# Kernel tuning notes

Hardware: AMD Instinct MI355X
Metric: run time of the kernel (lower is better)

Reference implementation:

```python
import jax, jax.numpy as jnp
import numpy as np

EMBED = 1024
N_HEAD = 16
B, T = 4, 2048


def setup_inputs() -> dict:
    key = jax.random.key(0)
    k1, k2, k3 = jax.random.split(key, 3)
    x = jax.random.normal(k1, (B, T, EMBED), dtype=jnp.float32)
    w_attn = jax.random.normal(k2, (EMBED, 3 * EMBED), dtype=jnp.float32) * 0.02
    w_proj = jax.random.normal(k3, (EMBED, EMBED), dtype=jnp.float32) * 0.02
    return {"x": x, "w_attn": w_attn, "w_proj": w_proj}


def reference(x, w_attn, w_proj):
    Bv, Tv, C = x.shape
    hd = C // N_HEAD
    qkv = x @ w_attn                      # [B,T,3C] (bias=False)
    q, k, v = jnp.split(qkv, 3, axis=-1)
    # [B,T,C] -> [B,H,T,hd]
    def heads(t):
        return t.reshape(Bv, Tv, N_HEAD, hd).transpose(0, 2, 1, 3)
    q, k, v = heads(q), heads(k), heads(v)
    att = jnp.einsum('bhqd,bhkd->bhqk', q, k) / jnp.sqrt(jnp.float32(hd))
    causal = jnp.tril(jnp.ones((Tv, Tv), dtype=bool))
    att = jnp.where(causal[None, None], att, -jnp.inf)
    att = jax.nn.softmax(att, axis=-1)    # dropout=0 (eval)
    y = jnp.einsum('bhqk,bhkd->bhqd', att, v)
    y = y.transpose(0, 2, 1, 3).reshape(Bv, Tv, C)
    return y @ w_proj
```

## Files before the change

kernel.cpp:

```cpp
#include <hip/hip_runtime.h>
#include <hip/hip_bf16.h>

typedef __attribute__((ext_vector_type(8))) short bf16x8;
typedef __attribute__((ext_vector_type(4))) float f32x4;

#define C1 0.180336880111112f

static __device__ __forceinline__ unsigned short f2bf(float f) {
    union { float f; unsigned int i; } u; u.f = f;
    unsigned int r = u.i + 0x7fffu + ((u.i >> 16) & 1u);
    return (unsigned short)(r >> 16);
}
static __device__ __forceinline__ unsigned int cvt_pk_bf16(float lo, float hi) {
    unsigned int r;
    asm("v_cvt_pk_bf16_f32 %0, %1, %2" : "=v"(r) : "v"(lo), "v"(hi));
    return r;
}

__global__ __launch_bounds__(256)
void prep_kernel(const float* __restrict__ x, const float* __restrict__ wA, const float* __restrict__ wP,
                 unsigned short* __restrict__ xb, unsigned short* __restrict__ wtA,
                 unsigned short* __restrict__ wtP) {
    const int bid = blockIdx.x, tid = threadIdx.x;
    if (bid < 2048) {
        int i0 = bid * 256 + tid;
        #pragma unroll
        for (int it = 0; it < 4; ++it) {
            int i = i0 + it * 524288;
            float4 v = reinterpret_cast<const float4*>(x)[i];
            ushort4 o;
            o.x = f2bf(v.x); o.y = f2bf(v.y); o.z = f2bf(v.z); o.w = f2bf(v.w);
            reinterpret_cast<ushort4*>(xb)[i] = o;
        }
    } else {
        const float* in; unsigned short* out; int R, C, bx, by;
        if (bid < 5120) { int l = bid - 2048; in = wA; out = wtA; R = 1024; C = 3072; bx = l % 96; by = l / 96; }
        else            { int l = bid - 5120; in = wP; out = wtP; R = 1024; C = 1024; bx = l % 32; by = l / 32; }
        __shared__ float tile[32][33];
        const int c0 = bx * 32, r0 = by * 32;
        const int tx = tid & 31, ty = tid >> 5;
        #pragma unroll
        for (int i = 0; i < 32; i += 8)
            tile[ty + i][tx] = in[(size_t)(r0 + ty + i) * C + c0 + tx];
        __syncthreads();
        #pragma unroll
        for (int i = 0; i < 32; i += 8)
            out[(size_t)(c0 + ty + i) * R + r0 + tx] = f2bf(tile[tx][ty + i]);
    }
}

template<int MODE>
__global__ __launch_bounds__(256, 4)
void gemm_bt2(const unsigned short* __restrict__ A,
              const unsigned short* __restrict__ B,
              void* __restrict__ Cout,
              int M, int N, int K) {
    __shared__ unsigned short As[8192];
    __shared__ unsigned short Bs[8192];
    const int tid = threadIdx.x;
    const int wave = tid >> 6, lane = tid & 63;
    const int wr = wave >> 1, wc = wave & 1;
    const int lg = lane >> 4, lr = lane & 15;
    const int m0 = blockIdx.y * 128, n0 = blockIdx.x * 128;

    const int slot = tid * 16;
    const int srow = slot >> 7;
    const int scol = ((slot & 127) ^ ((srow & 7) << 4)) >> 1;
    const int swz = (lr & 7) << 4;

    f32x4 acc[4][4] = {};

    for (int kt = 0; kt < K; kt += 64) {
        #pragma unroll
        for (int i = 0; i < 4; ++i) {
            __builtin_amdgcn_global_load_lds(
                (const __attribute__((address_space(1))) void*)(A + (size_t)(m0 + i * 32 + srow) * K + kt + scol),
                (__attribute__((address_space(3))) void*)(As + ((i * 4096 + slot) >> 1)), 16, 0, 0);
            __builtin_amdgcn_global_load_lds(
                (const __attribute__((address_space(1))) void*)(B + (size_t)(n0 + i * 32 + srow) * K + kt + scol),
                (__attribute__((address_space(3))) void*)(Bs + ((i * 4096 + slot) >> 1)), 16, 0, 0);
        }
        __syncthreads();
        #pragma unroll
        for (int kk = 0; kk < 2; ++kk) {
            bf16x8 af[4], bfr[4];
            #pragma unroll
            for (int mi = 0; mi < 4; ++mi)
                af[mi] = *reinterpret_cast<const bf16x8*>(
                    (const char*)As + (wr * 64 + mi * 16 + lr) * 128 + ((kk * 64 + lg * 16) ^ swz));
            #pragma unroll
            for (int ni = 0; ni < 4; ++ni)
                bfr[ni] = *reinterpret_cast<const bf16x8*>(
                    (const char*)Bs + (wc * 64 + ni * 16 + lr) * 128 + ((kk * 64 + lg * 16) ^ swz));
            #pragma unroll
            for (int mi = 0; mi < 4; ++mi)
                #pragma unroll
                for (int ni = 0; ni < 4; ++ni)
                    acc[mi][ni] = __builtin_amdgcn_mfma_f32_16x16x32_bf16(af[mi], bfr[ni], acc[mi][ni], 0, 0, 0);
        }
        __syncthreads();
    }

    if (MODE == 0) {
        float* C = (float*)Cout;
        #pragma unroll
        for (int mi = 0; mi < 4; ++mi)
            #pragma unroll
            for (int ni = 0; ni < 4; ++ni)
                #pragma unroll
                for (int r = 0; r < 4; ++r) {
                    int row = m0 + wr * 64 + mi * 16 + lg * 4 + r;
                    int col = n0 + wc * 64 + ni * 16 + lr;
                    C[(size_t)row * N + col] = acc[mi][ni][r];
                }
    } else {
        unsigned short* QKV = (unsigned short*)Cout;
        #pragma unroll
        for (int mi = 0; mi < 4; ++mi) {
            int rowb = m0 + wr * 64 + mi * 16 + lg * 4;
            int bb = rowb >> 11, t = rowb & 2047;
            #pragma unroll
            for (int ni = 0; ni < 4; ++ni) {
                int col = n0 + wc * 64 + ni * 16 + lr;
                int which = col >> 10;
                int hh = (col & 1023) >> 6;
                int d = col & 63;
                int bhh = bb * 16 + hh;
                if (which == 2) {
                    ushort4 o;
                    o.x = f2bf(acc[mi][ni][0]); o.y = f2bf(acc[mi][ni][1]);
                    o.z = f2bf(acc[mi][ni][2]); o.w = f2bf(acc[mi][ni][3]);
                    *reinterpret_cast<ushort4*>(QKV + (size_t)2 * 8388608 +
                                                ((size_t)bhh * 64 + d) * 2048 + t) = o;
                } else {
                    #pragma unroll
                    for (int r = 0; r < 4; ++r)
                        QKV[(size_t)which * 8388608 +
                            ((size_t)bhh * 2048 + t + r) * 64 + d] = f2bf(acc[mi][ni][r]);
                }
            }
        }
    }
}

__global__ __launch_bounds__(256)
void attn_fwd(const unsigned short* __restrict__ Qb,
              const unsigned short* __restrict__ Kb,
              const unsigned short* __restrict__ Vtb,
              unsigned short* __restrict__ Yb) {
    const int bh = blockIdx.x;
    const int qt = 15 - (int)blockIdx.y;
    const int tid = threadIdx.x;
    const int wave = tid >> 6, lane = tid & 63;
    const int lg = lane >> 4, lr = lane & 15;
    const int b = bh >> 4, h = bh & 15;

    __shared__ unsigned short Ks[2][4096];
    __shared__ unsigned short Vs[2][4096];
    __shared__ unsigned short Ps[4][32][72];

    const unsigned short* Qh = Qb + (size_t)bh * (2048 * 64);
    const unsigned short* Kh = Kb + (size_t)bh * (2048 * 64);
    const unsigned short* Vh = Vtb + (size_t)bh * (64 * 2048);

    const int slot = tid * 16;
    const int srow = slot >> 7;
    const int scol = ((slot & 127) ^ ((srow & 7) << 4)) >> 1;

    const int swz = (lr & 7) << 4;
    const short one_bf = (short)0x3F80;
    const bf16x8 onesv = {one_bf, one_bf, one_bf, one_bf, one_bf, one_bf, one_bf, one_bf};

#define STAGE(bb, kv)                                                                              \
    {                                                                                              \
        _Pragma("unroll")                                                                          \
        for (int i_ = 0; i_ < 2; ++i_) {                                                           \
            __builtin_amdgcn_global_load_lds(                                                      \
                (const __attribute__((address_space(1))) void*)(Kh + (size_t)((kv) + i_ * 32 + srow) * 64 + scol), \
                (__attribute__((address_space(3))) void*)(Ks[bb] + ((i_ * 4096 + slot) >> 1)), 16, 0, 0); \
            __builtin_amdgcn_global_load_lds(                                                      \
                (const __attribute__((address_space(1))) void*)(Vh + (size_t)(i_ * 32 + srow) * 2048 + (kv) + scol), \
                (__attribute__((address_space(3))) void*)(Vs[bb] + ((i_ * 4096 + slot) >> 1)), 16, 0, 0); \
        }                                                                                          \
    }

    const int q0 = qt * 128;
    const int wq0 = q0 + wave * 32;

    bf16x8 qf[2][2];
    #pragma unroll
    for (int mi = 0; mi < 2; ++mi)
        #pragma unroll
        for (int kk = 0; kk < 2; ++kk)
            qf[mi][kk] = *reinterpret_cast<const bf16x8*>(
                Qh + (size_t)(wq0 + mi * 16 + lr) * 64 + kk * 32 + lg * 8);

    f32x4 oacc[4][2] = {};
    f32x4 sumacc[2] = {};
    float mst[2] = {-1e30f, -1e30f};

    const int nt = 2 * qt + 2;
    int cur = 0;

    STAGE(cur, 0);
    asm volatile("s_waitcnt vmcnt(0)" ::: "memory");
    __syncthreads();

    #pragma unroll 1
    for (int t = 0; t < nt; ++t) {
        const int kv0 = t << 6;
        if (t + 1 < nt) STAGE(cur ^ 1, kv0 + 64);

        if (kv0 < wq0 + 32) {
            const unsigned short* Kc = Ks[cur];
            const unsigned short* Vc = Vs[cur];

            f32x4 sacc[2][4] = {};
            __builtin_amdgcn_s_setprio(1);
            #pragma unroll
            for (int kk = 0; kk < 2; ++kk) {
                bf16x8 kf[4];
                #pragma unroll
                for (int ni = 0; ni < 4; ++ni)
                    kf[ni] = *reinterpret_cast<const bf16x8*>(
                        (const char*)Kc + (ni * 16 + lr) * 128 + ((kk * 64 + lg * 16) ^ swz));
                #pragma unroll
                for (int mi = 0; mi < 2; ++mi)
                    #pragma unroll
                    for (int ni = 0; ni < 4; ++ni)
                        sacc[mi][ni] = __builtin_amdgcn_mfma_f32_16x16x32_bf16(kf[ni], qf[mi][kk], sacc[mi][ni], 0, 0, 0);
            }
            __builtin_amdgcn_s_setprio(0);

            if (kv0 + 64 > wq0) {
                #pragma unroll
                for (int mi = 0; mi < 2; ++mi)
                    #pragma unroll
                    for (int ni = 0; ni < 4; ++ni)
                        #pragma unroll
                        for (int r = 0; r < 4; ++r) {
                            int k = kv0 + ni * 16 + lg * 4 + r;
                            int q = wq0 + mi * 16 + lr;
                            if (k > q) sacc[mi][ni][r] = -1e30f;
                        }
            }

            #pragma unroll
            for (int mi = 0; mi < 2; ++mi) {
                float m0v = fmaxf(fmaxf(sacc[mi][0][0], sacc[mi][0][1]), fmaxf(sacc[mi][0][2], sacc[mi][0][3]));
                float m1v = fmaxf(fmaxf(sacc[mi][1][0], sacc[mi][1][1]), fmaxf(sacc[mi][1][2], sacc[mi][1][3]));
                float m2v = fmaxf(fmaxf(sacc[mi][2][0], sacc[mi][2][1]), fmaxf(sacc[mi][2][2], sacc[mi][2][3]));
                float m3v = fmaxf(fmaxf(sacc[mi][3][0], sacc[mi][3][1]), fmaxf(sacc[mi][3][2], sacc[mi][3][3]));
                float mx = fmaxf(fmaxf(m0v, m1v), fmaxf(m2v, m3v));
                mx = fmaxf(mx, __shfl_xor(mx, 16));
                mx = fmaxf(mx, __shfl_xor(mx, 32));

                if (!__all(mx <= mst[mi] + 64.0f)) {
                    float mnew = fmaxf(mst[mi], mx);
                    float alpha = __builtin_amdgcn_exp2f((mst[mi] - mnew) * C1);
                    mst[mi] = mnew;
                    sumacc[mi] *= alpha;
                    #pragma unroll
                    for (int nd = 0; nd < 4; ++nd)
                        oacc[nd][mi] *= alpha;
                }
                float mc = mst[mi] * C1;
                #pragma unroll
                for (int ni = 0; ni < 4; ++ni)
                    #pragma unroll
                    for (int r = 0; r < 4; ++r)
                        sacc[mi][ni][r] = __builtin_amdgcn_exp2f(__builtin_fmaf(sacc[mi][ni][r], C1, -mc));

                #pragma unroll
                for (int ni = 0; ni < 4; ++ni) {
                    uint2 w;
                    w.x = cvt_pk_bf16(sacc[mi][ni][0], sacc[mi][ni][1]);
                    w.y = cvt_pk_bf16(sacc[mi][ni][2], sacc[mi][ni][3]);
                    *reinterpret_cast<uint2*>(&Ps[wave][mi * 16 + lr][ni * 16 + lg * 4]) = w;
                }
            }

            __builtin_amdgcn_s_setprio(1);
            #pragma unroll
            for (int ks = 0; ks < 2; ++ks) {
                bf16x8 pf[2], vf[4];
                #pragma unroll
                for (int mi = 0; mi < 2; ++mi)
                    pf[mi] = *reinterpret_cast<const bf16x8*>(&Ps[wave][mi * 16 + lr][ks * 32 + lg * 8]);
                #pragma unroll
                for (int nd = 0; nd < 4; ++nd)
                    vf[nd] = *reinterpret_cast<const bf16x8*>(
                        (const char*)Vc + (nd * 16 + lr) * 128 + ((ks * 64 + lg * 16) ^ swz));
                #pragma unroll
                for (int mi = 0; mi < 2; ++mi) {
                    sumacc[mi] = __builtin_amdgcn_mfma_f32_16x16x32_bf16(onesv, pf[mi], sumacc[mi], 0, 0, 0);
                    #pragma unroll
                    for (int nd = 0; nd < 4; ++nd)
                        oacc[nd][mi] = __builtin_amdgcn_mfma_f32_16x16x32_bf16(vf[nd], pf[mi], oacc[nd][mi], 0, 0, 0);
                }
            }
            __builtin_amdgcn_s_setprio(0);
        }

        asm volatile("s_waitcnt vmcnt(0)" ::: "memory");
        __syncthreads();
        cur ^= 1;
    }

    #pragma unroll
    for (int mi = 0; mi < 2; ++mi) {
        float rinv = __builtin_amdgcn_rcpf(sumacc[mi][0]);
        int tq = wq0 + mi * 16 + lr;
        size_t base = (((size_t)(b * 2048 + tq)) * 16 + h) * 64 + lg * 4;
        #pragma unroll
        for (int nd = 0; nd < 4; ++nd) {
            uint2 w;
            w.x = cvt_pk_bf16(oacc[nd][mi][0] * rinv, oacc[nd][mi][1] * rinv);
            w.y = cvt_pk_bf16(oacc[nd][mi][2] * rinv, oacc[nd][mi][3] * rinv);
            *reinterpret_cast<uint2*>(Yb + base + nd * 16) = w;
        }
    }
#undef STAGE
}

extern "C" void kernel_launch(void* const* d_in, const int* in_sizes, int n_in,
                              void* d_out, int out_size, void* d_ws, size_t ws_size,
                              hipStream_t stream) {
    const float* x      = (const float*)d_in[0];
    const float* w_attn = (const float*)d_in[1];
    const float* w_proj = (const float*)d_in[2];
    float* out = (float*)d_out;

    unsigned short* xb  = (unsigned short*)d_ws;
    unsigned short* wtA = xb  + 8388608;
    unsigned short* wtP = wtA + 3145728;
    unsigned short* qkv = wtP + 1048576;
    unsigned short* yb  = qkv + 3 * 8388608;

    prep_kernel<<<6144, 256, 0, stream>>>(x, w_attn, w_proj, xb, wtA, wtP);

    gemm_bt2<1><<<dim3(3072 / 128, 8192 / 128), 256, 0, stream>>>(xb, wtA, qkv, 8192, 3072, 1024);

    attn_fwd<<<dim3(64, 16), 256, 0, stream>>>(qkv, qkv + 8388608, qkv + 2 * 8388608, yb);

    gemm_bt2<0><<<dim3(1024 / 128, 8192 / 128), 256, 0, stream>>>(yb, wtP, out, 8192, 1024, 1024);
}
```

Before: 161.8 us.

## Load K and V fragments directly from global memory instead of LDS staging

Drops the double-buffered LDS staging of K and V tiles, which used global_load_lds, and the per-tile block barriers. Each wave now reads its K and V MFMA fragments straight from global memory and loops only over the KV tiles it needs. This removes the barrier synchronisation and the extra waiting caused by the causal imbalance between waves. In exchange the four waves no longer share tiles, so each one issues its own uncoalesced global loads, and there is no prefetch to hide that latency.

```diff
diff --git a/kernel.cpp b/kernel.cpp
--- a/kernel.cpp
+++ b/kernel.cpp
@@ -155,34 +155,14 @@
     const int lg = lane >> 4, lr = lane & 15;
     const int b = bh >> 4, h = bh & 15;
 
-    __shared__ unsigned short Ks[2][4096];
-    __shared__ unsigned short Vs[2][4096];
     __shared__ unsigned short Ps[4][32][72];
 
     const unsigned short* Qh = Qb + (size_t)bh * (2048 * 64);
     const unsigned short* Kh = Kb + (size_t)bh * (2048 * 64);
     const unsigned short* Vh = Vtb + (size_t)bh * (64 * 2048);
 
-    const int slot = tid * 16;
-    const int srow = slot >> 7;
-    const int scol = ((slot & 127) ^ ((srow & 7) << 4)) >> 1;
-
-    const int swz = (lr & 7) << 4;
     const short one_bf = (short)0x3F80;
     const bf16x8 onesv = {one_bf, one_bf, one_bf, one_bf, one_bf, one_bf, one_bf, one_bf};
-
-#define STAGE(bb, kv)                                                                              \
-    {                                                                                              \
-        _Pragma("unroll")                                                                          \
-        for (int i_ = 0; i_ < 2; ++i_) {                                                           \
-            __builtin_amdgcn_global_load_lds(                                                      \
-                (const __attribute__((address_space(1))) void*)(Kh + (size_t)((kv) + i_ * 32 + srow) * 64 + scol), \
-                (__attribute__((address_space(3))) void*)(Ks[bb] + ((i_ * 4096 + slot) >> 1)), 16, 0, 0); \
-            __builtin_amdgcn_global_load_lds(                                                      \
-                (const __attribute__((address_space(1))) void*)(Vh + (size_t)(i_ * 32 + srow) * 2048 + (kv) + scol), \
-                (__attribute__((address_space(3))) void*)(Vs[bb] + ((i_ * 4096 + slot) >> 1)), 16, 0, 0); \
-        }                                                                                          \
-    }
 
     const int q0 = qt * 128;
     const int wq0 = q0 + wave * 32;
@@ -199,112 +179,97 @@
     f32x4 sumacc[2] = {};
     float mst[2] = {-1e30f, -1e30f};
 
-    const int nt = 2 * qt + 2;
-    int cur = 0;
-
-    STAGE(cur, 0);
-    asm volatile("s_waitcnt vmcnt(0)" ::: "memory");
-    __syncthreads();
+    const int ntw = (wq0 + 32 + 63) >> 6;
 
     #pragma unroll 1
-    for (int t = 0; t < nt; ++t) {
+    for (int t = 0; t < ntw; ++t) {
         const int kv0 = t << 6;
-        if (t + 1 < nt) STAGE(cur ^ 1, kv0 + 64);
-
-        if (kv0 < wq0 + 32) {
-            const unsigned short* Kc = Ks[cur];
-            const unsigned short* Vc = Vs[cur];
-
-            f32x4 sacc[2][4] = {};
-            __builtin_amdgcn_s_setprio(1);
-            #pragma unroll
-            for (int kk = 0; kk < 2; ++kk) {
-                bf16x8 kf[4];
+
+        f32x4 sacc[2][4] = {};
+        __builtin_amdgcn_s_setprio(1);
+        #pragma unroll
+        for (int kk = 0; kk < 2; ++kk) {
+            bf16x8 kf[4];
+            #pragma unroll
+            for (int ni = 0; ni < 4; ++ni)
+                kf[ni] = *reinterpret_cast<const bf16x8*>(
+                    Kh + (size_t)(kv0 + ni * 16 + lr) * 64 + kk * 32 + lg * 8);
+            #pragma unroll
+            for (int mi = 0; mi < 2; ++mi)
                 #pragma unroll
                 for (int ni = 0; ni < 4; ++ni)
-                    kf[ni] = *reinterpret_cast<const bf16x8*>(
-                        (const char*)Kc + (ni * 16 + lr) * 128 + ((kk * 64 + lg * 16) ^ swz));
-                #pragma unroll
-                for (int mi = 0; mi < 2; ++mi)
-                    #pragma unroll
-                    for (int ni = 0; ni < 4; ++ni)
-                        sacc[mi][ni] = __builtin_amdgcn_mfma_f32_16x16x32_bf16(kf[ni], qf[mi][kk], sacc[mi][ni], 0, 0, 0);
-            }
-            __builtin_amdgcn_s_setprio(0);
-
-            if (kv0 + 64 > wq0) {
-                #pragma unroll
-                for (int mi = 0; mi < 2; ++mi)
-                    #pragma unroll
-                    for (int ni = 0; ni < 4; ++ni)
-                        #pragma unroll
-                        for (int r = 0; r < 4; ++r) {
-                            int k = kv0 + ni * 16 + lg * 4 + r;
-                            int q = wq0 + mi * 16 + lr;
-                            if (k > q) sacc[mi][ni][r] = -1e30f;
-                        }
-            }
-
-            #pragma unroll
-            for (int mi = 0; mi < 2; ++mi) {
-                float m0v = fmaxf(fmaxf(sacc[mi][0][0], sacc[mi][0][1]), fmaxf(sacc[mi][0][2], sacc[mi][0][3]));
-                float m1v = fmaxf(fmaxf(sacc[mi][1][0], sacc[mi][1][1]), fmaxf(sacc[mi][1][2], sacc[mi][1][3]));
-                float m2v = fmaxf(fmaxf(sacc[mi][2][0], sacc[mi][2][1]), fmaxf(sacc[mi][2][2], sacc[mi][2][3]));
-                float m3v = fmaxf(fmaxf(sacc[mi][3][0], sacc[mi][3][1]), fmaxf(sacc[mi][3][2], sacc[mi][3][3]));
-                float mx = fmaxf(fmaxf(m0v, m1v), fmaxf(m2v, m3v));
-                mx = fmaxf(mx, __shfl_xor(mx, 16));
-                mx = fmaxf(mx, __shfl_xor(mx, 32));
-
-                if (!__all(mx <= mst[mi] + 64.0f)) {
-                    float mnew = fmaxf(mst[mi], mx);
-                    float alpha = __builtin_amdgcn_exp2f((mst[mi] - mnew) * C1);
-                    mst[mi] = mnew;
-                    sumacc[mi] *= alpha;
-                    #pragma unroll
-                    for (int nd = 0; nd < 4; ++nd)
-                        oacc[nd][mi] *= alpha;
-                }
-                float mc = mst[mi] * C1;
+                    sacc[mi][ni] = __builtin_amdgcn_mfma_f32_16x16x32_bf16(kf[ni], qf[mi][kk], sacc[mi][ni], 0, 0, 0);
+        }
+        __builtin_amdgcn_s_setprio(0);
+
+        if (kv0 + 64 > wq0) {
+            #pragma unroll
+            for (int mi = 0; mi < 2; ++mi)
                 #pragma unroll
                 for (int ni = 0; ni < 4; ++ni)
                     #pragma unroll
-                    for (int r = 0; r < 4; ++r)
-                        sacc[mi][ni][r] = __builtin_amdgcn_exp2f(__builtin_fmaf(sacc[mi][ni][r], C1, -mc));
-
-                #pragma unroll
-                for (int ni = 0; ni < 4; ++ni) {
-                    uint2 w;
-                    w.x = cvt_pk_bf16(sacc[mi][ni][0], sacc[mi][ni][1]);
-                    w.y = cvt_pk_bf16(sacc[mi][ni][2], sacc[mi][ni][3]);
-                    *reinterpret_cast<uint2*>(&Ps[wave][mi * 16 + lr][ni * 16 + lg * 4]) = w;
-                }
+                    for (int r = 0; r < 4; ++r) {
+                        int k = kv0 + ni * 16 + lg * 4 + r;
+                        int q = wq0 + mi * 16 + lr;
+                        if (k > q) sacc[mi][ni][r] = -1e30f;
+                    }
+        }
+
+        #pragma unroll
+        for (int mi = 0; mi < 2; ++mi) {
+            float m0v = fmaxf(fmaxf(sacc[mi][0][0], sacc[mi][0][1]), fmaxf(sacc[mi][0][2], sacc[mi][0][3]));
+            float m1v = fmaxf(fmaxf(sacc[mi][1][0], sacc[mi][1][1]), fmaxf(sacc[mi][1][2], sacc[mi][1][3]));
+            float m2v = fmaxf(fmaxf(sacc[mi][2][0], sacc[mi][2][1]), fmaxf(sacc[mi][2][2], sacc[mi][2][3]));
+            float m3v = fmaxf(fmaxf(sacc[mi][3][0], sacc[mi][3][1]), fmaxf(sacc[mi][3][2], sacc[mi][3][3]));
+            float mx = fmaxf(fmaxf(m0v, m1v), fmaxf(m2v, m3v));
+            mx = fmaxf(mx, __shfl_xor(mx, 16));
+            mx = fmaxf(mx, __shfl_xor(mx, 32));
+
+            if (!__all(mx <= mst[mi] + 64.0f)) {
+                float mnew = fmaxf(mst[mi], mx);
+                float alpha = __builtin_amdgcn_exp2f((mst[mi] - mnew) * C1);
+                mst[mi] = mnew;
+                sumacc[mi] *= alpha;
+                #pragma unroll
+                for (int nd = 0; nd < 4; ++nd)
+                    oacc[nd][mi] *= alpha;
             }
-
-            __builtin_amdgcn_s_setprio(1);
-            #pragma unroll
-            for (int ks = 0; ks < 2; ++ks) {
-                bf16x8 pf[2], vf[4];
-                #pragma unroll
-                for (int mi = 0; mi < 2; ++mi)
-                    pf[mi] = *reinterpret_cast<const bf16x8*>(&Ps[wave][mi * 16 + lr][ks * 32 + lg * 8]);
+            float mc = mst[mi] * C1;
+            #pragma unroll
+            for (int ni = 0; ni < 4; ++ni)
+                #pragma unroll
+                for (int r = 0; r < 4; ++r)
+                    sacc[mi][ni][r] = __builtin_amdgcn_exp2f(__builtin_fmaf(sacc[mi][ni][r], C1, -mc));
+
+            #pragma unroll
+            for (int ni = 0; ni < 4; ++ni) {
+                uint2 w;
+                w.x = cvt_pk_bf16(sacc[mi][ni][0], sacc[mi][ni][1]);
+                w.y = cvt_pk_bf16(sacc[mi][ni][2], sacc[mi][ni][3]);
+                *reinterpret_cast<uint2*>(&Ps[wave][mi * 16 + lr][ni * 16 + lg * 4]) = w;
+            }
+        }
+
+        __builtin_amdgcn_s_setprio(1);
+        #pragma unroll
+        for (int ks = 0; ks < 2; ++ks) {
+            bf16x8 pf[2], vf[4];
+            #pragma unroll
+            for (int mi = 0; mi < 2; ++mi)
+                pf[mi] = *reinterpret_cast<const bf16x8*>(&Ps[wave][mi * 16 + lr][ks * 32 + lg * 8]);
+            #pragma unroll
+            for (int nd = 0; nd < 4; ++nd)
+                vf[nd] = *reinterpret_cast<const bf16x8*>(
+                    Vh + (size_t)(nd * 16 + lr) * 2048 + kv0 + ks * 32 + lg * 8);
+            #pragma unroll
+            for (int mi = 0; mi < 2; ++mi) {
+                sumacc[mi] = __builtin_amdgcn_mfma_f32_16x16x32_bf16(onesv, pf[mi], sumacc[mi], 0, 0, 0);
                 #pragma unroll
                 for (int nd = 0; nd < 4; ++nd)
-                    vf[nd] = *reinterpret_cast<const bf16x8*>(
-                        (const char*)Vc + (nd * 16 + lr) * 128 + ((ks * 64 + lg * 16) ^ swz));
-                #pragma unroll
-                for (int mi = 0; mi < 2; ++mi) {
-                    sumacc[mi] = __builtin_amdgcn_mfma_f32_16x16x32_bf16(onesv, pf[mi], sumacc[mi], 0, 0, 0);
-                    #pragma unroll
-                    for (int nd = 0; nd < 4; ++nd)
-                        oacc[nd][mi] = __builtin_amdgcn_mfma_f32_16x16x32_bf16(vf[nd], pf[mi], oacc[nd][mi], 0, 0, 0);
-                }
+                    oacc[nd][mi] = __builtin_amdgcn_mfma_f32_16x16x32_bf16(vf[nd], pf[mi], oacc[nd][mi], 0, 0, 0);
             }
-            __builtin_amdgcn_s_setprio(0);
-        }
-
-        asm volatile("s_waitcnt vmcnt(0)" ::: "memory");
-        __syncthreads();
-        cur ^= 1;
+        }
+        __builtin_amdgcn_s_setprio(0);
     }
 
     #pragma unroll
@@ -320,7 +285,6 @@
             *reinterpret_cast<uint2*>(Yb + base + nd * 16) = w;
         }
     }
-#undef STAGE
 }
 
 extern "C" void kernel_launch(void* const* d_in, const int* in_sizes, int n_in,
```

Result: slower. 213.8 us (+32.2%).
